# Optimization experiments

Measured on AMD Instinct MI355X. Metric: run time of the kernel, lower is better.

## Reference

```python
import jax, jax.numpy as jnp
import numpy as np

B, S, DIM_IN, DIM_K, DIM_V = 8, 4096, 1024, 128, 128


def setup_inputs() -> dict:
    key = jax.random.key(0)
    ks = jax.random.split(key, 9)
    s_in = 1.0 / np.sqrt(DIM_IN)
    return {
        "query": jax.random.normal(ks[0], (B, S, DIM_IN), jnp.float32),
        "key": jax.random.normal(ks[1], (B, S, DIM_IN), jnp.float32),
        "value": jax.random.normal(ks[2], (B, S, DIM_IN), jnp.float32),
        # Linear params stored as [in, out] (torch weight transposed)
        "Wq": jax.random.uniform(ks[3], (DIM_IN, DIM_K), jnp.float32, -s_in, s_in),
        "bq": jax.random.uniform(ks[4], (DIM_K,), jnp.float32, -s_in, s_in),
        "Wk": jax.random.uniform(ks[5], (DIM_IN, DIM_K), jnp.float32, -s_in, s_in),
        "bk": jax.random.uniform(ks[6], (DIM_K,), jnp.float32, -s_in, s_in),
        "Wv": jax.random.uniform(ks[7], (DIM_IN, DIM_V), jnp.float32, -s_in, s_in),
        "bv": jax.random.uniform(ks[8], (DIM_V,), jnp.float32, -s_in, s_in),
    }


def reference(query, key, value, Wq, bq, Wk, bk, Wv, bv):
    q = jnp.einsum("bsd,dk->bsk", query, Wq) + bq   # [B,S,DIM_K]
    k = jnp.einsum("bsd,dk->bsk", key, Wk) + bk     # [B,S,DIM_K]
    v = jnp.einsum("bsd,dv->bsv", value, Wv) + bv   # [B,S,DIM_V]
    scale = 1.0 / jnp.sqrt(jnp.asarray(q.shape[-1], q.dtype))
    scores = jnp.einsum("bqk,bsk->bqs", q, k) * scale  # [B,S,S]
    attn = jax.nn.softmax(scores, axis=-1)
    return jnp.einsum("bqs,bsv->bqv", attn, v)  # [B,S,DIM_V]
```

## Files before the change

### kernel.cpp

```cpp
#include <hip/hip_runtime.h>
#include <hip/hip_bf16.h>

typedef __attribute__((ext_vector_type(8))) short short8;
typedef __attribute__((ext_vector_type(4))) float f32x4;
typedef __attribute__((ext_vector_type(16))) float f32x16;
typedef __attribute__((ext_vector_type(4))) unsigned int u32x4;

#define MFMA32(A, B, C) __builtin_amdgcn_mfma_f32_32x32x16_bf16((A), (B), (C), 0, 0, 0)

__device__ __forceinline__ short f2bf(float x) {
  unsigned u = __float_as_uint(x);
  return (short)((u + 0x7FFFu + ((u >> 16) & 1u)) >> 16);
}

__device__ __forceinline__ unsigned cvtpk(float lo, float hi) {
  unsigned r;
  asm("v_cvt_pk_bf16_f32 %0, %1, %2" : "=v"(r) : "v"(lo), "v"(hi));
  return r;
}

__device__ __forceinline__ void gload16(const void* g, const void* s) {
  __builtin_amdgcn_global_load_lds(
      (const __attribute__((address_space(1))) unsigned int*)g,
      (__attribute__((address_space(3))) unsigned int*)s, 16, 0, 0);
}

__global__ __launch_bounds__(256) void wt_kernel(
    const float* __restrict__ Wq, const float* __restrict__ Wk, const float* __restrict__ Wv,
    short* __restrict__ WqT, short* __restrict__ WkT, short* __restrict__ WvT)
{
  const float* W  = (blockIdx.y == 0) ? Wq  : (blockIdx.y == 1) ? Wk  : Wv;
  short*       WT = (blockIdx.y == 0) ? WqT : (blockIdx.y == 1) ? WkT : WvT;
  int idx = blockIdx.x * 256 + threadIdx.x;
  int n = idx >> 10, k = idx & 1023;
  WT[idx] = f2bf(W[k * 128 + n]);
}

__global__ __launch_bounds__(256, 2) void proj_kernel(
    const float* __restrict__ Aq, const float* __restrict__ Ak, const float* __restrict__ Av,
    const short* __restrict__ WqT, const short* __restrict__ WkT, const short* __restrict__ WvT,
    const float* __restrict__ bq, const float* __restrict__ bk, const float* __restrict__ bv,
    short* __restrict__ Qs, short* __restrict__ Ks, short* __restrict__ VTs,
    float scale_q)
{
  __shared__ float lds[16384];
  const int y = blockIdx.y;
  const float* A    = (y == 0) ? Aq  : (y == 1) ? Ak  : Av;
  const short* WT   = (y == 0) ? WqT : (y == 1) ? WkT : WvT;
  const float* bias = (y == 0) ? bq  : (y == 1) ? bk  : bv;
  const int tid = threadIdx.x, l = tid & 63, w = tid >> 6;
  const int l31 = l & 31, hi = l >> 5;
  const long m0 = (long)blockIdx.x * 32;

  const float* A0 = A + m0 * 1024;
  int ag[8];
  #pragma unroll
  for (int i = 0; i < 8; ++i) {
    const int r_ = 8 * w + i;
    const int cb = (l * 16) ^ ((r_ & 15) << 4);
    ag[i] = r_ * 1024 + (cb >> 2);
  }

  #define ASTAGE(bb, kc) { \
    const float* s_ = A0 + (kc) * 256; \
    _Pragma("unroll") \
    for (int i = 0; i < 8; ++i) \
      gload16(s_ + ag[i], &lds[(bb) * 8192 + (8 * w + i) * 256]); \
  }

  f32x16 acc = {};
  const int n_ = w * 32 + l31;
  const short* Wn = WT + (long)n_ * 1024 + hi * 8;
  const char* abase = (const char*)lds;
  const int sw = (l31 & 15) << 4;

  ASTAGE(0, 0);

  for (int kc = 0; kc < 4; ++kc) {
    const int bb = kc & 1;
    short8 wb[16];
    #pragma unroll
    for (int k16 = 0; k16 < 16; ++k16)
      wb[k16] = *(const short8*)(Wn + kc * 256 + k16 * 16);
    if (kc + 1 < 4) {
      ASTAGE(bb ^ 1, kc + 1);
      asm volatile("s_waitcnt vmcnt(8)" ::: "memory");
    } else {
      asm volatile("s_waitcnt vmcnt(0)" ::: "memory");
    }
    __builtin_amdgcn_s_barrier();

    const char* ab = abase + bb * 32768 + l31 * 1024;
    if (y < 2) {
      #pragma unroll
      for (int k16 = 0; k16 < 16; ++k16) {
        const int c = k16 * 64 + hi * 32;
        f32x4 a0 = *(const f32x4*)(ab + ((c)      ^ sw));
        f32x4 a1 = *(const f32x4*)(ab + ((c + 16) ^ sw));
        short8 af;
        af[0] = f2bf(a0[0]); af[1] = f2bf(a0[1]); af[2] = f2bf(a0[2]); af[3] = f2bf(a0[3]);
        af[4] = f2bf(a1[0]); af[5] = f2bf(a1[1]); af[6] = f2bf(a1[2]); af[7] = f2bf(a1[3]);
        acc = MFMA32(af, wb[k16], acc);
      }
    } else {
      #pragma unroll
      for (int k16 = 0; k16 < 16; ++k16) {
        const int c = k16 * 64 + hi * 32;
        f32x4 a0 = *(const f32x4*)(ab + ((c)      ^ sw));
        f32x4 a1 = *(const f32x4*)(ab + ((c + 16) ^ sw));
        short8 af;
        af[0] = f2bf(a0[0]); af[1] = f2bf(a0[1]); af[2] = f2bf(a0[2]); af[3] = f2bf(a0[3]);
        af[4] = f2bf(a1[0]); af[5] = f2bf(a1[1]); af[6] = f2bf(a1[2]); af[7] = f2bf(a1[3]);
        acc = MFMA32(wb[k16], af, acc);
      }
    }
    asm volatile("s_waitcnt lgkmcnt(0)" ::: "memory");
    __builtin_amdgcn_s_barrier();
  }

  if (y < 2) {
    short* Out = (y == 0) ? Qs : Ks;
    const float sc = (y == 0) ? scale_q : 1.0f;
    const float bs = bias[n_];
    #pragma unroll
    for (int r = 0; r < 16; ++r) {
      const int row_ = (r & 3) + 8 * (r >> 2) + 4 * hi;
      Out[(m0 + row_) * 128 + n_] = f2bf((acc[r] + bs) * sc);
    }
  } else {
    #pragma unroll
    for (int r = 0; r < 16; ++r) {
      const int dv_ = w * 32 + (r & 3) + 8 * (r >> 2) + 4 * hi;
      VTs[(long)dv_ * 32768 + m0 + l31] = f2bf(acc[r] + bias[dv_]);
    }
  }
}

__global__ __launch_bounds__(256, 2) void attn_kernel(
    const short* __restrict__ Q,
    const short* __restrict__ K,
    const short* __restrict__ VT,
    float* __restrict__ O0,
    float* __restrict__ O1,
    float2* __restrict__ stats,
    int ntiles)
{
  __shared__ short lds[32768];
  const int tid = threadIdx.x, l = tid & 63, w = tid >> 6;
  const int l31 = l & 31, hi = l >> 5, xm = (l & 7) << 3;
  const int qb = blockIdx.x, h = blockIdx.y;
  const int b = qb >> 5;
  const int qrow = qb * 128 + w * 32 + l31;
  const long kv0 = (long)b * 4096 + (long)h * ntiles * 64;

  short8 qf[8];
  const short* Qp = Q + (long)qrow * 128 + hi * 8;
  #pragma unroll
  for (int ds = 0; ds < 8; ++ds) qf[ds] = *(const short8*)(Qp + ds * 16);

  const short* Kt = K + kv0 * 128;
  const short* Vt = VT + kv0;
  int kg_off[4]; long vg_off[4];
  #pragma unroll
  for (int r = 0; r < 4; ++r) {
    int c = r * 256 + tid;
    int p = c * 16;
    kg_off[r] = (p ^ (((p >> 8) & 7) << 4)) >> 1;
    int e = (p ^ (((p >> 7) & 7) << 4)) >> 1;
    vg_off[r] = (long)(e >> 6) * 32768 + (e & 63);
  }

  #define STAGE(bb, t) { \
    const short* kg_ = Kt + (t) * 8192; \
    const short* vg_ = Vt + (t) * 64; \
    _Pragma("unroll") \
    for (int r = 0; r < 4; ++r) { \
      gload16(kg_ + kg_off[r], &lds[(bb) * 16384 + r * 2048 + w * 512]); \
      gload16(vg_ + vg_off[r], &lds[(bb) * 16384 + 8192 + r * 2048 + w * 512]); \
    } }

  f32x16 acc0 = {}, acc1 = {}, acc2 = {}, acc3 = {};
  float m = -3e38f, lsum = 0.f;
  const int kread = l31 * 128;

  STAGE(0, 0);

  for (int t = 0; t < ntiles; ++t) {
    const int bb = t & 1;
    if (t + 1 < ntiles) {
      STAGE(bb ^ 1, t + 1);
      asm volatile("s_waitcnt vmcnt(8)" ::: "memory");
    } else {
      asm volatile("s_waitcnt vmcnt(0)" ::: "memory");
    }
    __builtin_amdgcn_s_barrier();

    const short* kb = &lds[bb * 16384];
    const short* vb = &lds[bb * 16384 + 8192];

    f32x16 st0 = {}, st1 = {};
    #pragma unroll
    for (int ds = 0; ds < 8; ++ds) {
      int co = (ds * 16 + hi * 8) ^ xm;
      short8 kf0 = *(const short8*)(kb + kread + co);
      short8 kf1 = *(const short8*)(kb + 4096 + kread + co);
      st0 = MFMA32(kf0, qf[ds], st0);
      st1 = MFMA32(kf1, qf[ds], st1);
    }

    float a0 = fmaxf(fmaxf(st0[0], st0[1]),  fmaxf(st0[2], st0[3]));
    float a1 = fmaxf(fmaxf(st0[4], st0[5]),  fmaxf(st0[6], st0[7]));
    float a2 = fmaxf(fmaxf(st0[8], st0[9]),  fmaxf(st0[10], st0[11]));
    float a3 = fmaxf(fmaxf(st0[12], st0[13]), fmaxf(st0[14], st0[15]));
    float b0 = fmaxf(fmaxf(st1[0], st1[1]),  fmaxf(st1[2], st1[3]));
    float b1 = fmaxf(fmaxf(st1[4], st1[5]),  fmaxf(st1[6], st1[7]));
    float b2 = fmaxf(fmaxf(st1[8], st1[9]),  fmaxf(st1[10], st1[11]));
    float b3 = fmaxf(fmaxf(st1[12], st1[13]), fmaxf(st1[14], st1[15]));
    float pm = fmaxf(fmaxf(fmaxf(a0, a1), fmaxf(a2, a3)),
                     fmaxf(fmaxf(b0, b1), fmaxf(b2, b3)));
    pm = fmaxf(pm, __shfl_xor(pm, 32));
    if (!__all(pm <= m + 8.f)) {
      float mn = fmaxf(m, pm);
      float al = exp2f(m - mn);
      m = mn;
      lsum *= al;
      acc0 *= al; acc1 *= al; acc2 *= al; acc3 *= al;
    }
    float ts = 0.f;
    #pragma unroll
    for (int j = 0; j < 16; ++j) { st0[j] = exp2f(st0[j] - m); ts += st0[j]; }
    #pragma unroll
    for (int j = 0; j < 16; ++j) { st1[j] = exp2f(st1[j] - m); ts += st1[j]; }
    ts += __shfl_xor(ts, 32);
    lsum += ts;

    unsigned pk[16];
    #pragma unroll
    for (int j = 0; j < 8; ++j) pk[j]     = cvtpk(st0[2 * j], st0[2 * j + 1]);
    #pragma unroll
    for (int j = 0; j < 8; ++j) pk[8 + j] = cvtpk(st1[2 * j], st1[2 * j + 1]);

    #pragma unroll
    for (int f = 0; f < 4; ++f) {
      auto r02 = __builtin_amdgcn_permlane32_swap(pk[f * 4 + 0], pk[f * 4 + 2], false, false);
      auto r13 = __builtin_amdgcn_permlane32_swap(pk[f * 4 + 1], pk[f * 4 + 3], false, false);
      union { u32x4 u; short8 s; } pf;
      pf.u = (u32x4){r02[0], r13[0], r02[1], r13[1]};
      int vo = (f * 16 + hi * 8) ^ xm;
      acc0 = MFMA32(*(const short8*)(vb +        l31 * 64 + vo), pf.s, acc0);
      acc1 = MFMA32(*(const short8*)(vb + 2048 + l31 * 64 + vo), pf.s, acc1);
      acc2 = MFMA32(*(const short8*)(vb + 4096 + l31 * 64 + vo), pf.s, acc2);
      acc3 = MFMA32(*(const short8*)(vb + 6144 + l31 * 64 + vo), pf.s, acc3);
    }

    asm volatile("s_waitcnt lgkmcnt(0)" ::: "memory");
    __builtin_amdgcn_s_barrier();
  }

  float* Op = ((h == 0) ? O0 : O1) + (long)qrow * 128;
  #define STORE_DT(A, dtb) { \
    _Pragma("unroll") \
    for (int jj = 0; jj < 4; ++jj) { \
      f32x4 o_ = {A[4 * jj], A[4 * jj + 1], A[4 * jj + 2], A[4 * jj + 3]}; \
      *(f32x4*)(Op + (dtb) + jj * 8 + hi * 4) = o_; \
    } }
  STORE_DT(acc0, 0) STORE_DT(acc1, 32) STORE_DT(acc2, 64) STORE_DT(acc3, 96)

  if (l < 32) stats[(long)h * 32768 + qrow] = make_float2(m, lsum);
}

__global__ __launch_bounds__(256) void merge_kernel(
    float* __restrict__ O, const float* __restrict__ O1,
    const float2* __restrict__ stats, int halves)
{
  int idx = blockIdx.x * 256 + threadIdx.x;
  int q = idx >> 5, c = (idx & 31) * 4;
  long off = (long)q * 128 + c;
  float2 s0 = stats[q];
  f32x4 a = *(const f32x4*)(O + off);
  if (halves == 2) {
    float2 s1 = stats[32768 + q];
    float M = fmaxf(s0.x, s1.x);
    float w0 = exp2f(s0.x - M), w1 = exp2f(s1.x - M);
    f32x4 bv = *(const f32x4*)(O1 + off);
    float inv = 1.f / (w0 * s0.y + w1 * s1.y);
    a = (a * w0 + bv * w1) * inv;
  } else {
    a = a * (1.f / s0.y);
  }
  *(f32x4*)(O + off) = a;
}

extern "C" void kernel_launch(void* const* d_in, const int* in_sizes, int n_in,
                              void* d_out, int out_size, void* d_ws, size_t ws_size,
                              hipStream_t stream) {
  const float* query = (const float*)d_in[0];
  const float* key   = (const float*)d_in[1];
  const float* value = (const float*)d_in[2];
  const float* Wq = (const float*)d_in[3];
  const float* bq = (const float*)d_in[4];
  const float* Wk = (const float*)d_in[5];
  const float* bk = (const float*)d_in[6];
  const float* Wv = (const float*)d_in[7];
  const float* bv = (const float*)d_in[8];

  char* wsb = (char*)d_ws;
  short* Qs  = (short*)(wsb);
  short* Ks  = (short*)(wsb + 8388608);
  short* VTs = (short*)(wsb + 16777216);
  short* WqT = (short*)(wsb + 25165824);
  short* WkT = (short*)(wsb + 25427968);
  short* WvT = (short*)(wsb + 25690112);
  float* O1  = (float*)(wsb + 25952256);
  const size_t NEED2 = 25952256ull + 16777216ull + 524288ull;
  int halves = (ws_size >= NEED2) ? 2 : 1;
  float2* stats = (float2*)(wsb + (halves == 2 ? 42729472ull : 25952256ull));
  int ntiles = (halves == 2) ? 32 : 64;

  wt_kernel<<<dim3(512, 3), 256, 0, stream>>>(Wq, Wk, Wv, WqT, WkT, WvT);
  const float scale_q = 0.08838834764831845f * 1.4426950408889634f;
  proj_kernel<<<dim3(1024, 3), 256, 0, stream>>>(query, key, value, WqT, WkT, WvT,
                                                 bq, bk, bv, Qs, Ks, VTs, scale_q);
  attn_kernel<<<dim3(256, halves), 256, 0, stream>>>(Qs, Ks, VTs, (float*)d_out, O1, stats, ntiles);
  merge_kernel<<<4096, 256, 0, stream>>>((float*)d_out, O1, stats, halves);
}
```

Baseline: 248.0 us.

## Stage projection activations through registers, converting to bf16 before LDS

The projection kernel stops using direct global-to-LDS loads of fp32 activations. Each thread now loads fp32 chunks into registers with nontemporal loads, packs them to bf16 with v_cvt_pk, and writes them to a half-size swizzled LDS buffer. MFMA operands then come straight from bf16 LDS, and weights are loaded per k-step instead of prefetched into a 16-register array. The smaller LDS footprint and fewer registers allow four blocks per CU instead of two, at the cost of register-staged prefetching and a vmcnt(0) stall before each LDS write.

```diff
diff --git a/kernel.cpp b/kernel.cpp
--- a/kernel.cpp
+++ b/kernel.cpp
@@ -36,14 +36,14 @@
   WT[idx] = f2bf(W[k * 128 + n]);
 }
 
-__global__ __launch_bounds__(256, 2) void proj_kernel(
+__global__ __launch_bounds__(256, 4) void proj_kernel(
     const float* __restrict__ Aq, const float* __restrict__ Ak, const float* __restrict__ Av,
     const short* __restrict__ WqT, const short* __restrict__ WkT, const short* __restrict__ WvT,
     const float* __restrict__ bq, const float* __restrict__ bk, const float* __restrict__ bv,
     short* __restrict__ Qs, short* __restrict__ Ks, short* __restrict__ VTs,
     float scale_q)
 {
-  __shared__ float lds[16384];
+  __shared__ short lds[16384];
   const int y = blockIdx.y;
   const float* A    = (y == 0) ? Aq  : (y == 1) ? Ak  : Av;
   const short* WT   = (y == 0) ? WqT : (y == 1) ? WkT : WvT;
@@ -52,67 +52,76 @@
   const int l31 = l & 31, hi = l >> 5;
   const long m0 = (long)blockIdx.x * 32;
 
-  const float* A0 = A + m0 * 1024;
-  int ag[8];
-  #pragma unroll
-  for (int i = 0; i < 8; ++i) {
-    const int r_ = 8 * w + i;
-    const int cb = (l * 16) ^ ((r_ & 15) << 4);
-    ag[i] = r_ * 1024 + (cb >> 2);
-  }
-
-  #define ASTAGE(bb, kc) { \
-    const float* s_ = A0 + (kc) * 256; \
+  const int srow = w * 2 + (l >> 5);
+  const int scol = (l & 31) * 8;
+  const float* As = A + (m0 + srow) * 1024 + scol;
+  const int swb = ((l & 31) * 16);
+
+  f32x4 sa0, sa1, sa2, sa3, sb0, sb1, sb2, sb3;
+
+  #define PISSUE() { \
+    sa0 = __builtin_nontemporal_load((const f32x4*)(Asx));        \
+    sb0 = __builtin_nontemporal_load((const f32x4*)(Asx + 4));    \
+    sa1 = __builtin_nontemporal_load((const f32x4*)(Asx + 8192)); \
+    sb1 = __builtin_nontemporal_load((const f32x4*)(Asx + 8196)); \
+    sa2 = __builtin_nontemporal_load((const f32x4*)(Asx + 16384));\
+    sb2 = __builtin_nontemporal_load((const f32x4*)(Asx + 16388));\
+    sa3 = __builtin_nontemporal_load((const f32x4*)(Asx + 24576));\
+    sb3 = __builtin_nontemporal_load((const f32x4*)(Asx + 24580));}
+
+  #define PWRITE(bb) { \
     _Pragma("unroll") \
-    for (int i = 0; i < 8; ++i) \
-      gload16(s_ + ag[i], &lds[(bb) * 8192 + (8 * w + i) * 256]); \
-  }
+    for (int rr = 0; rr < 4; ++rr) { \
+      const f32x4 va = (rr == 0) ? sa0 : (rr == 1) ? sa1 : (rr == 2) ? sa2 : sa3; \
+      const f32x4 vb = (rr == 0) ? sb0 : (rr == 1) ? sb1 : (rr == 2) ? sb2 : sb3; \
+      u32x4 pk_; \
+      pk_[0] = cvtpk(va[0], va[1]); pk_[1] = cvtpk(va[2], va[3]); \
+      pk_[2] = cvtpk(vb[0], vb[1]); pk_[3] = cvtpk(vb[2], vb[3]); \
+      const int r_ = rr * 8 + srow; \
+      *(u32x4*)((char*)lds + (bb) * 16384 + r_ * 512 + (swb ^ ((r_ & 15) << 4))) = pk_; \
+    } }
 
   f32x16 acc = {};
   const int n_ = w * 32 + l31;
   const short* Wn = WT + (long)n_ * 1024 + hi * 8;
-  const char* abase = (const char*)lds;
-  const int sw = (l31 & 15) << 4;
-
-  ASTAGE(0, 0);
-
+  const char* ab0 = (const char*)lds + l31 * 512;
+  const int swz = (l31 & 15) << 4;
+
+  {
+    const float* Asx = As;
+    PISSUE();
+    asm volatile("s_waitcnt vmcnt(0)" ::: "memory");
+    PWRITE(0);
+    asm volatile("s_waitcnt lgkmcnt(0)" ::: "memory");
+    __builtin_amdgcn_s_barrier();
+  }
+
+  #pragma unroll
   for (int kc = 0; kc < 4; ++kc) {
     const int bb = kc & 1;
-    short8 wb[16];
-    #pragma unroll
-    for (int k16 = 0; k16 < 16; ++k16)
-      wb[k16] = *(const short8*)(Wn + kc * 256 + k16 * 16);
     if (kc + 1 < 4) {
-      ASTAGE(bb ^ 1, kc + 1);
-      asm volatile("s_waitcnt vmcnt(8)" ::: "memory");
-    } else {
-      asm volatile("s_waitcnt vmcnt(0)" ::: "memory");
-    }
-    __builtin_amdgcn_s_barrier();
-
-    const char* ab = abase + bb * 32768 + l31 * 1024;
+      const float* Asx = As + (kc + 1) * 256;
+      PISSUE();
+    }
+    const char* ab = ab0 + bb * 16384;
     if (y < 2) {
       #pragma unroll
       for (int k16 = 0; k16 < 16; ++k16) {
-        const int c = k16 * 64 + hi * 32;
-        f32x4 a0 = *(const f32x4*)(ab + ((c)      ^ sw));
-        f32x4 a1 = *(const f32x4*)(ab + ((c + 16) ^ sw));
-        short8 af;
-        af[0] = f2bf(a0[0]); af[1] = f2bf(a0[1]); af[2] = f2bf(a0[2]); af[3] = f2bf(a0[3]);
-        af[4] = f2bf(a1[0]); af[5] = f2bf(a1[1]); af[6] = f2bf(a1[2]); af[7] = f2bf(a1[3]);
-        acc = MFMA32(af, wb[k16], acc);
+        short8 af = *(const short8*)(ab + ((k16 * 32 + hi * 16) ^ swz));
+        short8 wb = *(const short8*)(Wn + kc * 256 + k16 * 16);
+        acc = MFMA32(af, wb, acc);
       }
     } else {
       #pragma unroll
       for (int k16 = 0; k16 < 16; ++k16) {
-        const int c = k16 * 64 + hi * 32;
-        f32x4 a0 = *(const f32x4*)(ab + ((c)      ^ sw));
-        f32x4 a1 = *(const f32x4*)(ab + ((c + 16) ^ sw));
-        short8 af;
-        af[0] = f2bf(a0[0]); af[1] = f2bf(a0[1]); af[2] = f2bf(a0[2]); af[3] = f2bf(a0[3]);
-        af[4] = f2bf(a1[0]); af[5] = f2bf(a1[1]); af[6] = f2bf(a1[2]); af[7] = f2bf(a1[3]);
-        acc = MFMA32(wb[k16], af, acc);
+        short8 af = *(const short8*)(ab + ((k16 * 32 + hi * 16) ^ swz));
+        short8 wb = *(const short8*)(Wn + kc * 256 + k16 * 16);
+        acc = MFMA32(wb, af, acc);
       }
+    }
+    if (kc + 1 < 4) {
+      asm volatile("s_waitcnt vmcnt(0)" ::: "memory");
+      PWRITE(bb ^ 1);
     }
     asm volatile("s_waitcnt lgkmcnt(0)" ::: "memory");
     __builtin_amdgcn_s_barrier();
```

After: 691.7 us. 179% more time.
